# Performance work log

Measured on AMD Instinct MI355X. Metric: run time of the kernel, lower is better.

Reference implementation:

```python
import jax, jax.numpy as jnp
import numpy as np

# NOTE: the original source calls an undefined selective_scan_fn(x, delta, A_bar, B_bar, C)
# and returns y_proj(y). We implement the standard S6 diagonal selective scan it implies:
#   h_t = A_bar_t * h_{t-1} + B_bar_t * u_t   (elementwise over latent dim, h_0 = 0)
#   y_t = C_t * h_t
# with u = x_proj(x) (the only use of the otherwise-dangling x_proj in the source).

IN_CH = 96
OUT_CH = 96
LATENT = 256
BATCH, H, W = 2, 128, 128


def _linear(x, w, b):
    return x @ w.T + b


def _s6(x, xw, xb, bcw, bcb, dw, db, yw, yb):
    # x: [B, L, Cin]
    u = _linear(x, xw, xb)                      # [B, L, D]
    bc = _linear(x, bcw, bcb)                   # [B, L, 2D]
    delta = _linear(x, dw, db)                  # [B, L, D]
    Bm, Cm = jnp.split(bc, 2, axis=-1)
    A_bar = jnp.exp(-jax.nn.softplus(delta))    # in (0, 1)
    B_bar = (1.0 - A_bar) * Bm
    elems = (A_bar, B_bar * u)

    def combine(c1, c2):
        a1, b1 = c1
        a2, b2 = c2
        return (a1 * a2, a2 * b1 + b2)

    _, h = jax.lax.associative_scan(combine, elems, axis=1)  # parallel scan over L
    y = Cm * h
    return _linear(y, yw, yb)                   # [B, L, D]


def setup_inputs() -> dict:
    key = jax.random.key(0)
    ks = jax.random.split(key, 16)
    s = 0.02
    inp = {
        "x": jax.random.normal(ks[0], (BATCH, IN_CH, H, W), jnp.float32),
        # S6 params (shared across all 4 directional scans, as in the source)
        "xw": jax.random.normal(ks[1], (LATENT, IN_CH), jnp.float32) * s,
        "xb": jnp.zeros((LATENT,), jnp.float32),
        "bcw": jax.random.normal(ks[2], (2 * LATENT, IN_CH), jnp.float32) * s,
        "bcb": jnp.zeros((2 * LATENT,), jnp.float32),
        "dw": jax.random.normal(ks[3], (LATENT, IN_CH), jnp.float32) * s,
        "db": jnp.zeros((LATENT,), jnp.float32),
        "yw": jax.random.normal(ks[4], (LATENT, LATENT), jnp.float32) * s,
        "yb": jnp.zeros((LATENT,), jnp.float32),
        # CrossMerge params
        "mw": jax.random.normal(ks[5], (LATENT, 4 * LATENT), jnp.float32) * s,
        "mb": jnp.zeros((LATENT,), jnp.float32),
        "gw": jax.random.normal(ks[6], (LATENT, 4 * LATENT), jnp.float32) * s,
        "gb": jnp.zeros((LATENT,), jnp.float32),
        "ow": jax.random.normal(ks[7], (OUT_CH, LATENT), jnp.float32) * s,
        "ob": jnp.zeros((OUT_CH,), jnp.float32),
    }
    return inp


def reference(x, xw, xb, bcw, bcb, dw, db, yw, yb, mw, mb, gw, gb, ow, ob):
    B, C, Hh, Ww = x.shape
    # cross_scan: 4 directional flattenings
    s1 = x.transpose(0, 2, 3, 1).reshape(B, Hh * Ww, C)   # 'b c h w -> b (h w) c'
    s2 = x.transpose(0, 3, 2, 1).reshape(B, Ww * Hh, C)   # 'b c h w -> b (w h) c'
    s3 = s1[:, ::-1, :]
    s4 = s2[:, ::-1, :]
    p = (xw, xb, bcw, bcb, dw, db, yw, yb)
    y1 = _s6(s1, *p)
    y2 = _s6(s2, *p)
    y3 = _s6(s3, *p)
    y4 = _s6(s4, *p)
    # CrossMerge
    y_cat = jnp.concatenate([y1, y2, y3, y4], axis=-1)    # [B, L, 4D]
    y_merged = _linear(y_cat, mw, mb)
    gate = jax.nn.sigmoid(_linear(y_cat, gw, gb))
    out = _linear(y_merged * gate, ow, ob)                # [B, L, OUT_CH]
    # 'b (h w) c -> b c h w'
    return out.reshape(B, Hh, Ww, -1).transpose(0, 3, 1, 2)
```

## Files before the change

kernel.cpp:

```cpp
#include <hip/hip_runtime.h>
#include <stdint.h>

#define LL 16384
#define NB 2
#define CIN 96
#define NLAT 256
#define COUT 96
#define NCH 256
#define CHU 64

typedef __attribute__((ext_vector_type(8))) short short8v;
typedef __attribute__((ext_vector_type(4))) float float4v;

__device__ __forceinline__ float b2f(unsigned short h) {
    return __uint_as_float(((unsigned int)h) << 16);
}
__device__ __forceinline__ unsigned short f2b(float f) {
    unsigned int u = __float_as_uint(f);
    unsigned int r = (u + 0x7FFFu + ((u >> 16) & 1u)) >> 16;
    return (unsigned short)r;
}

#define GLL16(g, s) __builtin_amdgcn_global_load_lds( \
    (const __attribute__((address_space(1))) unsigned int*)(g), \
    (__attribute__((address_space(3))) unsigned int*)(s), 16, 0, 0)

__global__ __launch_bounds__(256) void k_foldw_part(
    const float* __restrict__ yw, const float* __restrict__ mw, const float* __restrict__ gw,
    float* __restrict__ WF)
{
    __shared__ float At[64][68];
    __shared__ float Bt[64][68];
    int jt = blockIdx.x, nt = blockIdx.y, dzk = blockIdx.z;
    int kc = dzk & 3, dz = dzk >> 2;
    int d = dz & 3, mat = dz >> 2;
    const float* src = mat ? gw : mw;
    int j0 = jt * 64, n0 = nt * 64;
    int tid = threadIdx.x, tx = tid & 15, ty = tid >> 4;
    float acc[4][4] = {};
    int i0 = kc * 64;
    for (int rep = 0; rep < 16; ++rep) {
        int idx = rep * 256 + tid;
        int r = idx >> 6, cq = idx & 63;
        At[r][cq] = yw[(size_t)(i0 + r) * 256 + j0 + cq];
        Bt[cq][r] = src[(size_t)(n0 + r) * 1024 + d * 256 + i0 + cq];
    }
    __syncthreads();
    for (int ii = 0; ii < 64; ++ii) {
        float4 a4 = *(const float4*)(&At[ii][ty * 4]);
        float4 b4 = *(const float4*)(&Bt[ii][tx * 4]);
        float av[4] = {a4.x, a4.y, a4.z, a4.w};
        float bv[4] = {b4.x, b4.y, b4.z, b4.w};
        for (int q = 0; q < 4; ++q)
            for (int p = 0; p < 4; ++p)
                acc[q][p] = fmaf(av[q], bv[p], acc[q][p]);
    }
    float* dst = WF + (size_t)kc * 512 * 1024;
    for (int q = 0; q < 4; ++q) {
        int k = d * 256 + j0 + ty * 4 + q;
        for (int p = 0; p < 4; ++p) {
            int n = n0 + tx * 4 + p;
            dst[(size_t)(mat * 256 + n) * 1024 + k] = acc[q][p];
        }
    }
}

__global__ __launch_bounds__(256) void k_foldsum(
    const float* __restrict__ WF, unsigned short* __restrict__ WBT)
{
    int t = blockIdx.x * 256 + threadIdx.x;
    size_t o = (size_t)t * 4;
    const size_t S = (size_t)512 * 1024;
    float4 s0 = *(const float4*)(WF + o);
    float4 s1 = *(const float4*)(WF + S + o);
    float4 s2 = *(const float4*)(WF + 2 * S + o);
    float4 s3 = *(const float4*)(WF + 3 * S + o);
    unsigned short pk[4];
    pk[0] = f2b(s0.x + s1.x + s2.x + s3.x);
    pk[1] = f2b(s0.y + s1.y + s2.y + s3.y);
    pk[2] = f2b(s0.z + s1.z + s2.z + s3.z);
    pk[3] = f2b(s0.w + s1.w + s2.w + s3.w);
    *(unsigned long long*)(&WBT[o]) = *(const unsigned long long*)pk;
}

__global__ void k_foldbias(const float* __restrict__ mw, const float* __restrict__ gw,
                           const float* __restrict__ mb, const float* __restrict__ gb,
                           const float* __restrict__ yb,
                           float* __restrict__ bm2, float* __restrict__ bg2)
{
    int row = blockIdx.x;
    int lane = threadIdx.x;
    int n = row & 255;
    const float* W = (row < 256) ? mw : gw;
    float s = 0.f;
    for (int k = lane; k < 1024; k += 64)
        s = fmaf(W[(size_t)n * 1024 + k], yb[k & 255], s);
    for (int off = 32; off; off >>= 1) s += __shfl_down(s, off);
    if (lane == 0) {
        if (row < 256) bm2[n] = s + mb[n];
        else           bg2[n] = s + gb[n];
    }
}

__global__ __launch_bounds__(256) void k_xpose(
    const float* __restrict__ x, unsigned short* __restrict__ XT)
{
    int t = threadIdx.x;
    int pl = t & 63;
    int grp = t >> 6;
    int p0 = blockIdx.x * 64;
    int b = p0 >> 14;
    int l = (p0 & (LL - 1)) + pl;
    size_t gp = (size_t)(p0 + pl);
    const float* xr = x + (size_t)b * 96 * LL + l;
    unsigned short* orow = XT + gp * 192;
#pragma unroll
    for (int kk = 0; kk < 3; ++kk) {
        int kq = grp * 3 + kk;
        short8v hi, lo;
#pragma unroll
        for (int c = 0; c < 8; ++c) {
            float v = xr[(size_t)(kq * 8 + c) * LL];
            unsigned short h = f2b(v);
            float r = v - b2f(h);
            hi[c] = (short)h;
            lo[c] = (short)f2b(r);
        }
        *(short8v*)(orow + kq * 8) = hi;
        *(short8v*)(orow + 96 + kq * 8) = lo;
    }
}

__global__ void k_wprep(
    const float* __restrict__ xw, const float* __restrict__ bcw, const float* __restrict__ dw,
    unsigned short* __restrict__ WPT)
{
    int rp = blockIdx.x * 32 + (threadIdx.x >> 3);
    int sub = threadIdx.x & 7;
    int nn16 = rp >> 6, g = (rp >> 4) & 3, ni = rp & 15;
    int n = nn16 * 16 + ni;
    const float* row;
    if (g == 0)      row = xw + (size_t)n * 96;
    else if (g == 1) row = bcw + (size_t)n * 96;
    else if (g == 2) row = bcw + (size_t)(256 + n) * 96;
    else             row = dw + (size_t)n * 96;
    unsigned short* orow = WPT + (size_t)rp * 192;
    for (int kq = sub; kq < 12; kq += 8) {
        short8v hv;
#pragma unroll
        for (int c = 0; c < 8; ++c) hv[c] = (short)f2b(row[kq * 8 + c]);
        *(short8v*)(orow + kq * 8) = hv;
        *(short8v*)(orow + 96 + kq * 8) = hv;
    }
}

__global__ void k_owprep(const float* __restrict__ ow, unsigned short* __restrict__ OWB)
{
    int r = blockIdx.x;
    int lane = threadIdx.x;
    unsigned short pk[4];
    if (r < 96) {
        float4 v = *(const float4*)(ow + (size_t)r * 256 + lane * 4);
        pk[0] = f2b(v.x); pk[1] = f2b(v.y); pk[2] = f2b(v.z); pk[3] = f2b(v.w);
    } else {
        pk[0] = pk[1] = pk[2] = pk[3] = 0;
    }
    *(unsigned long long*)(&OWB[(size_t)r * 256 + lane * 4]) = *(const unsigned long long*)pk;
}

__global__ __launch_bounds__(256) void k_proj_mfma(
    const unsigned short* __restrict__ XT, const unsigned short* __restrict__ WPT,
    const float* __restrict__ xb, const float* __restrict__ bcb, const float* __restrict__ db,
    unsigned int* __restrict__ AB, unsigned short* __restrict__ C)
{
    __shared__ __align__(16) unsigned short smA[128 * 32];
    __shared__ __align__(16) unsigned short smB[128 * 32];
    int tid = threadIdx.x;
    int w = tid >> 6, l = tid & 63;
    int mt = blockIdx.x;
    int bnt = blockIdx.y;
    int p0 = mt * 128;
    int bn0 = bnt * 128;

    int rowA = tid >> 2;
    int chA  = tid & 3;
    int laneRow = l & 15;
    int laneK   = l >> 4;

    float4v acc[2][8];
#pragma unroll
    for (int i = 0; i < 2; ++i)
#pragma unroll
        for (int f = 0; f < 8; ++f) acc[i][f] = (float4v)0.f;

    for (int kt = 0; kt < 6; ++kt) {
        const unsigned short* gA = XT + (size_t)(p0 + rowA) * 192 + kt * 32 + chA * 8;
        const unsigned short* gB = WPT + (size_t)(bn0 + rowA) * 192 + kt * 32 + chA * 8;
        GLL16(gA,            smA + tid * 8);
        GLL16(gA + 64 * 192, smA + 2048 + tid * 8);
        GLL16(gB,            smB + tid * 8);
        GLL16(gB + 64 * 192, smB + 2048 + tid * 8);
        __syncthreads();

        short8v a0 = *(const short8v*)(&smA[(w * 32 + laneRow) * 32 + laneK * 8]);
        short8v a1 = *(const short8v*)(&smA[(w * 32 + 16 + laneRow) * 32 + laneK * 8]);
#pragma unroll
        for (int f = 0; f < 8; ++f) {
            short8v bf_ = *(const short8v*)(&smB[(f * 16 + laneRow) * 32 + laneK * 8]);
            acc[0][f] = __builtin_amdgcn_mfma_f32_16x16x32_bf16(a0, bf_, acc[0][f], 0, 0, 0);
            acc[1][f] = __builtin_amdgcn_mfma_f32_16x16x32_bf16(a1, bf_, acc[1][f], 0, 0, 0);
        }
        __syncthreads();
    }

    int lr = l >> 4, lc = l & 15;
#pragma unroll
    for (int mr = 0; mr < 2; ++mr) {
#pragma unroll
        for (int nn2 = 0; nn2 < 2; ++nn2) {
            int n = (bnt * 2 + nn2) * 16 + lc;
            float xbv = xb[n], bb = bcb[n], cb = bcb[256 + n], dbv = db[n];
#pragma unroll
            for (int q = 0; q < 4; ++q) {
                int p = p0 + w * 32 + mr * 16 + lr * 4 + q;
                float u  = acc[mr][nn2 * 4 + 0][q] + xbv;
                float Bm = acc[mr][nn2 * 4 + 1][q] + bb;
                float Cm = acc[mr][nn2 * 4 + 2][q] + cb;
                float dl = acc[mr][nn2 * 4 + 3][q] + dbv;
                float a  = 1.0f / (1.0f + __expf(dl));
                float bu = (1.0f - a) * Bm * u;
                size_t base = (size_t)p * NLAT + n;
                AB[base] = (unsigned int)f2b(a) | ((unsigned int)f2b(bu) << 16);
                C[base]  = f2b(Cm);
            }
        }
    }
}

__device__ __forceinline__ int src_pos(int d, int t) {
    int s = (d >= 2) ? (LL - 1 - t) : t;
    return (d & 1) ? (((s & 127) << 7) | (s >> 7)) : s;
}

__global__ __launch_bounds__(256) void k_scan1(
    const unsigned int* __restrict__ AB,
    float* __restrict__ AggA, float* __restrict__ AggB)
{
    int n = threadIdx.x;
    int c = blockIdx.x, dp = blockIdx.y, b = blockIdx.z;
    int d1 = dp, d2 = dp + 2;
    int c2 = NCH - 1 - c;
    int t01 = c * CHU, t02 = c2 * CHU;
    const unsigned int* ABb = AB + (size_t)b * LL * NLAT + n;
    float h1 = 0.f, A1 = 1.f, h2 = 0.f, A2 = 1.f;
#pragma unroll 4
    for (int i = 0; i < CHU; ++i) {
        int ls1 = src_pos(d1, t01 + i);
        int ls2 = src_pos(d2, t02 + i);
        unsigned int v1 = ABb[(size_t)ls1 * NLAT];
        unsigned int v2 = ABb[(size_t)ls2 * NLAT];
        float a1 = __uint_as_float(v1 << 16), bu1 = __uint_as_float(v1 & 0xFFFF0000u);
        float a2 = __uint_as_float(v2 << 16), bu2 = __uint_as_float(v2 & 0xFFFF0000u);
        h1 = fmaf(a1, h1, bu1); A1 *= a1;
        h2 = fmaf(a2, h2, bu2); A2 *= a2;
    }
    size_t o1 = (((size_t)b * 4 + d1) * NCH + c) * NLAT + n;
    size_t o2 = (((size_t)b * 4 + d2) * NCH + c2) * NLAT + n;
    AggA[o1] = A1; AggB[o1] = h1;
    AggA[o2] = A2; AggB[o2] = h2;
}

__global__ void k_scan2(const float* __restrict__ AggA, const float* __restrict__ AggB,
                        float* __restrict__ Hs)
{
    int n = threadIdx.x;
    int d = blockIdx.x, b = blockIdx.y;
    float h = 0.f;
    for (int c = 0; c < NCH; ++c) {
        size_t o = (((size_t)b * 4 + d) * NCH + c) * NLAT + n;
        Hs[o] = h;
        h = fmaf(AggA[o], h, AggB[o]);
    }
}

__global__ __launch_bounds__(256) void k_scan3(
    const unsigned int* __restrict__ AB, const unsigned short* __restrict__ C,
    const float* __restrict__ Hs, unsigned short* __restrict__ ys)
{
    int n = threadIdx.x;
    int c = blockIdx.x, dp = blockIdx.y, b = blockIdx.z;
    int d1 = dp, d2 = dp + 2;
    int c2 = NCH - 1 - c;
    int t01 = c * CHU, t02 = c2 * CHU;
    const unsigned int* ABb = AB + (size_t)b * LL * NLAT + n;
    const unsigned short* Cb = C + (size_t)b * LL * NLAT + n;
    size_t o1 = (((size_t)b * 4 + d1) * NCH + c) * NLAT + n;
    size_t o2 = (((size_t)b * 4 + d2) * NCH + c2) * NLAT + n;
    float h1 = Hs[o1], h2 = Hs[o2];
    size_t yb1 = (((size_t)b * 4 + d1) * LL + t01) * NLAT + n;
    size_t yb2 = (((size_t)b * 4 + d2) * LL + t02) * NLAT + n;
#pragma unroll 4
    for (int i = 0; i < CHU; ++i) {
        int ls1 = src_pos(d1, t01 + i);
        int ls2 = src_pos(d2, t02 + i);
        size_t i1 = (size_t)ls1 * NLAT, i2 = (size_t)ls2 * NLAT;
        unsigned int v1 = ABb[i1];
        unsigned int v2 = ABb[i2];
        float a1 = __uint_as_float(v1 << 16), bu1 = __uint_as_float(v1 & 0xFFFF0000u);
        float a2 = __uint_as_float(v2 << 16), bu2 = __uint_as_float(v2 & 0xFFFF0000u);
        h1 = fmaf(a1, h1, bu1);
        h2 = fmaf(a2, h2, bu2);
        float y1 = b2f(Cb[i1]) * h1;
        float y2 = b2f(Cb[i2]) * h2;
        ys[yb1 + (size_t)i * NLAT] = f2b(y1);
        ys[yb2 + (size_t)i * NLAT] = f2b(y2);
    }
}

__global__ __launch_bounds__(256) void k_merge_mfma(
    const unsigned short* __restrict__ ys,
    const unsigned short* __restrict__ WBT,
    const float* __restrict__ bm2, const float* __restrict__ bg2,
    unsigned short* __restrict__ z)
{
    __shared__ __align__(16) unsigned short smA[2 * 128 * 32];
    __shared__ __align__(16) unsigned short smB[2 * 256 * 32];
    int tid = threadIdx.x;
    int w = tid >> 6, l = tid & 63;
    int wm = w >> 1, wn = w & 1;
    int mt = blockIdx.x;
    int nt = blockIdx.y;
    int p0 = mt * 128;
    int b4 = (p0 >> 14) * 4;
    int l0 = p0 & (LL - 1);
    int n0 = nt * 128;

    int rS = tid >> 2;
    int cg = (tid & 3) ^ ((rS >> 1) & 3);
    int laneRow = l & 15;
    int laneK   = l >> 4;
    int rx = (laneRow >> 1) & 3;

    float4v accM[4][4], accG[4][4];
#pragma unroll
    for (int i = 0; i < 4; ++i)
#pragma unroll
        for (int j = 0; j < 4; ++j) { accM[i][j] = (float4v)0.f; accG[i][j] = (float4v)0.f; }

    auto stage = [&](int kt, int buf) {
        int d = kt >> 3;
        int j0k = (kt & 7) * 32;
        const unsigned short* gAb = ys + (((size_t)(b4 + d)) * LL + l0) * 256 + j0k + cg * 8;
        unsigned short* sA = smA + buf * 4096;
        unsigned short* sB = smB + buf * 8192;
#pragma unroll
        for (int rep = 0; rep < 2; ++rep) {
            GLL16(gAb + (size_t)(rep * 64 + rS) * 256, sA + rep * 2048 + tid * 8);
        }
#pragma unroll
        for (int rep = 0; rep < 4; ++rep) {
            int rr = rep * 64 + rS;
            int nrow = (rr < 128) ? (n0 + rr) : (256 + n0 + rr - 128);
            GLL16(WBT + (size_t)nrow * 1024 + kt * 32 + cg * 8, sB + rep * 2048 + tid * 8);
        }
    };

    stage(0, 0);

    int cur = 0;
    for (int kt = 0; kt < 32; ++kt) {
        if (kt < 31) {
            stage(kt + 1, cur ^ 1);
            asm volatile("s_waitcnt vmcnt(6)" ::: "memory");
        } else {
            asm volatile("s_waitcnt vmcnt(0)" ::: "memory");
        }
        __builtin_amdgcn_s_barrier();

        const unsigned short* sA = smA + cur * 4096;
        const unsigned short* sB = smB + cur * 8192;
        int cxo = (laneK ^ rx) * 8;
        short8v a[4];
#pragma unroll
        for (int mr = 0; mr < 4; ++mr)
            a[mr] = *(const short8v*)(&sA[(wm * 64 + mr * 16 + laneRow) * 32 + cxo]);
#pragma unroll
        for (int nr = 0; nr < 4; ++nr) {
            short8v bm_ = *(const short8v*)(&sB[(wn * 64 + nr * 16 + laneRow) * 32 + cxo]);
            short8v bg_ = *(const short8v*)(&sB[(128 + wn * 64 + nr * 16 + laneRow) * 32 + cxo]);
#pragma unroll
            for (int mr = 0; mr < 4; ++mr) {
                accM[mr][nr] = __builtin_amdgcn_mfma_f32_16x16x32_bf16(a[mr], bm_, accM[mr][nr], 0, 0, 0);
                accG[mr][nr] = __builtin_amdgcn_mfma_f32_16x16x32_bf16(a[mr], bg_, accG[mr][nr], 0, 0, 0);
            }
        }
        __builtin_amdgcn_s_barrier();
        cur ^= 1;
    }

    int lr = l >> 4, lc = l & 15;
#pragma unroll
    for (int mr = 0; mr < 4; ++mr) {
#pragma unroll
        for (int nr = 0; nr < 4; ++nr) {
            int n = n0 + wn * 64 + nr * 16 + lc;
            float bmv = bm2[n], bgv = bg2[n];
#pragma unroll
            for (int q = 0; q < 4; ++q) {
                int p = p0 + wm * 64 + mr * 16 + lr * 4 + q;
                float m = accM[mr][nr][q] + bmv;
                float g = accG[mr][nr][q] + bgv;
                float zv = m / (1.f + __expf(-g));
                z[(size_t)p * NLAT + n] = f2b(zv);
            }
        }
    }
}

__global__ __launch_bounds__(256) void k_out_mfma(
    const unsigned short* __restrict__ z, const unsigned short* __restrict__ OWB,
    const float* __restrict__ ob, float* __restrict__ out)
{
    __shared__ __align__(16) unsigned short smA[128 * 32];
    __shared__ __align__(16) unsigned short smB[128 * 32];
    int tid = threadIdx.x;
    int w = tid >> 6, l = tid & 63;
    int p0 = blockIdx.x * 128;
    int b = p0 >> 14;
    int l0 = p0 & (LL - 1);

    int rowA = tid >> 2;
    int chA  = tid & 3;
    int laneRow = l & 15;
    int laneK   = l >> 4;

    float4v acc[2][6];
#pragma unroll
    for (int i = 0; i < 2; ++i)
#pragma unroll
        for (int f = 0; f < 6; ++f) acc[i][f] = (float4v)0.f;

    for (int kt = 0; kt < 8; ++kt) {
        const unsigned short* gA = z + (size_t)(p0 + rowA) * 256 + kt * 32 + chA * 8;
        const unsigned short* gB = OWB + (size_t)rowA * 256 + kt * 32 + chA * 8;
        GLL16(gA,            smA + tid * 8);
        GLL16(gA + 64 * 256, smA + 2048 + tid * 8);
        GLL16(gB,            smB + tid * 8);
        GLL16(gB + 64 * 256, smB + 2048 + tid * 8);
        __syncthreads();

        short8v a0 = *(const short8v*)(&smA[(w * 32 + laneRow) * 32 + laneK * 8]);
        short8v a1 = *(const short8v*)(&smA[(w * 32 + 16 + laneRow) * 32 + laneK * 8]);
#pragma unroll
        for (int nr = 0; nr < 6; ++nr) {
            short8v bf_ = *(const short8v*)(&smB[(nr * 16 + laneRow) * 32 + laneK * 8]);
            acc[0][nr] = __builtin_amdgcn_mfma_f32_16x16x32_bf16(a0, bf_, acc[0][nr], 0, 0, 0);
            acc[1][nr] = __builtin_amdgcn_mfma_f32_16x16x32_bf16(a1, bf_, acc[1][nr], 0, 0, 0);
        }
        __syncthreads();
    }

    int lr = l >> 4, lc = l & 15;
#pragma unroll
    for (int mr = 0; mr < 2; ++mr) {
#pragma unroll
        for (int nr = 0; nr < 6; ++nr) {
            int c = nr * 16 + lc;
            float obv = ob[c];
            int ll = l0 + w * 32 + mr * 16 + lr * 4;
            float4 v;
            v.x = acc[mr][nr][0] + obv;
            v.y = acc[mr][nr][1] + obv;
            v.z = acc[mr][nr][2] + obv;
            v.w = acc[mr][nr][3] + obv;
            *(float4*)(&out[((size_t)(b * 96 + c)) * LL + ll]) = v;
        }
    }
}

extern "C" void kernel_launch(void* const* d_in, const int* in_sizes, int n_in,
                              void* d_out, int out_size, void* d_ws, size_t ws_size,
                              hipStream_t stream) {
    (void)in_sizes; (void)n_in; (void)out_size; (void)ws_size;
    const float* x   = (const float*)d_in[0];
    const float* xw  = (const float*)d_in[1];
    const float* xb  = (const float*)d_in[2];
    const float* bcw = (const float*)d_in[3];
    const float* bcb = (const float*)d_in[4];
    const float* dw  = (const float*)d_in[5];
    const float* db  = (const float*)d_in[6];
    const float* yw  = (const float*)d_in[7];
    const float* yb  = (const float*)d_in[8];
    const float* mw  = (const float*)d_in[9];
    const float* mb  = (const float*)d_in[10];
    const float* gw  = (const float*)d_in[11];
    const float* gb  = (const float*)d_in[12];
    const float* ow  = (const float*)d_in[13];
    const float* ob  = (const float*)d_in[14];
    float* out = (float*)d_out;

    char* ws = (char*)d_ws;
    size_t off = 0;
    auto alloc = [&](size_t bytes) -> void* {
        void* p = ws + off;
        off += (bytes + 255) & ~(size_t)255;
        return p;
    };
    unsigned int*   AB  = (unsigned int*)  alloc((size_t)NB * LL * NLAT * 4);
    unsigned short* C   = (unsigned short*)alloc((size_t)NB * LL * NLAT * 2);
    unsigned short* YS  = (unsigned short*)alloc((size_t)NB * 4 * LL * NLAT * 2);
    unsigned short* Z   = (unsigned short*)alloc((size_t)NB * LL * NLAT * 2);
    unsigned short* WBT = (unsigned short*)alloc((size_t)512 * 1024 * 2);
    unsigned short* XT  = (unsigned short*)alloc((size_t)NB * LL * 192 * 2);
    unsigned short* WPT = (unsigned short*)alloc((size_t)1024 * 192 * 2);
    unsigned short* OWB = (unsigned short*)alloc((size_t)128 * 256 * 2);
    float* WF   = (float*)alloc((size_t)4 * 512 * 1024 * 4);
    float* BM2  = (float*)alloc(256 * 4);
    float* BG2  = (float*)alloc(256 * 4);
    float* AggA = (float*)alloc((size_t)NB * 4 * NCH * NLAT * 4);
    float* AggB = (float*)alloc((size_t)NB * 4 * NCH * NLAT * 4);
    float* HS   = (float*)alloc((size_t)NB * 4 * NCH * NLAT * 4);

    k_foldw_part<<<dim3(4, 4, 32),   256, 0, stream>>>(yw, mw, gw, WF);
    k_foldsum   <<<512,              256, 0, stream>>>(WF, WBT);
    k_foldbias  <<<512,               64, 0, stream>>>(mw, gw, mb, gb, yb, BM2, BG2);
    k_wprep     <<<32,               256, 0, stream>>>(xw, bcw, dw, WPT);
    k_owprep    <<<128,               64, 0, stream>>>(ow, OWB);
    k_xpose     <<<512,              256, 0, stream>>>(x, XT);
    k_proj_mfma <<<dim3(256, 8),     256, 0, stream>>>(XT, WPT, xb, bcb, db, AB, C);
    k_scan1     <<<dim3(NCH, 2, NB), 256, 0, stream>>>(AB, AggA, AggB);
    k_scan2     <<<dim3(4, NB),      256, 0, stream>>>(AggA, AggB, HS);
    k_scan3     <<<dim3(NCH, 2, NB), 256, 0, stream>>>(AB, C, HS, YS);
    k_merge_mfma<<<dim3(256, 2),     256, 0, stream>>>(YS, WBT, BM2, BG2, Z);
    k_out_mfma  <<<256,              256, 0, stream>>>(Z, OWB, ob, out);
}
```

Baseline: 189.5 us.

## Merge prep kernels into one launch and parallelize chunk-carry scan

Four small preprocessing kernels (input transpose/split, projection weight prep, output weight prep, bias folding) are combined into one kernel that branches on block index, cutting three launches. The middle scan stage, which ran only 8 blocks with each thread looping serially over 256 chunks, now runs one block per (latent, direction, batch) and does a Hillis-Steele scan in shared memory. The new scan reads AggA/AggB with a stride of NLAT floats between threads, so its loads are uncoalesced, and it does log-depth work with many barriers.

```diff
diff --git a/kernel.cpp b/kernel.cpp
--- a/kernel.cpp
+++ b/kernel.cpp
@@ -83,89 +83,88 @@
     *(unsigned long long*)(&WBT[o]) = *(const unsigned long long*)pk;
 }
 
-__global__ void k_foldbias(const float* __restrict__ mw, const float* __restrict__ gw,
-                           const float* __restrict__ mb, const float* __restrict__ gb,
-                           const float* __restrict__ yb,
-                           float* __restrict__ bm2, float* __restrict__ bg2)
-{
-    int row = blockIdx.x;
-    int lane = threadIdx.x;
-    int n = row & 255;
-    const float* W = (row < 256) ? mw : gw;
-    float s = 0.f;
-    for (int k = lane; k < 1024; k += 64)
-        s = fmaf(W[(size_t)n * 1024 + k], yb[k & 255], s);
-    for (int off = 32; off; off >>= 1) s += __shfl_down(s, off);
-    if (lane == 0) {
-        if (row < 256) bm2[n] = s + mb[n];
-        else           bg2[n] = s + gb[n];
-    }
-}
-
-__global__ __launch_bounds__(256) void k_xpose(
-    const float* __restrict__ x, unsigned short* __restrict__ XT)
-{
+__global__ __launch_bounds__(256) void k_prep(
+    const float* __restrict__ x, unsigned short* __restrict__ XT,
+    const float* __restrict__ xw, const float* __restrict__ bcw, const float* __restrict__ dw,
+    unsigned short* __restrict__ WPT,
+    const float* __restrict__ ow, unsigned short* __restrict__ OWB,
+    const float* __restrict__ mw, const float* __restrict__ gw,
+    const float* __restrict__ mb, const float* __restrict__ gb,
+    const float* __restrict__ yb,
+    float* __restrict__ bm2, float* __restrict__ bg2)
+{
+    int bid = blockIdx.x;
     int t = threadIdx.x;
-    int pl = t & 63;
-    int grp = t >> 6;
-    int p0 = blockIdx.x * 64;
-    int b = p0 >> 14;
-    int l = (p0 & (LL - 1)) + pl;
-    size_t gp = (size_t)(p0 + pl);
-    const float* xr = x + (size_t)b * 96 * LL + l;
-    unsigned short* orow = XT + gp * 192;
-#pragma unroll
-    for (int kk = 0; kk < 3; ++kk) {
-        int kq = grp * 3 + kk;
-        short8v hi, lo;
-#pragma unroll
-        for (int c = 0; c < 8; ++c) {
-            float v = xr[(size_t)(kq * 8 + c) * LL];
-            unsigned short h = f2b(v);
-            float r = v - b2f(h);
-            hi[c] = (short)h;
-            lo[c] = (short)f2b(r);
-        }
-        *(short8v*)(orow + kq * 8) = hi;
-        *(short8v*)(orow + 96 + kq * 8) = lo;
-    }
-}
-
-__global__ void k_wprep(
-    const float* __restrict__ xw, const float* __restrict__ bcw, const float* __restrict__ dw,
-    unsigned short* __restrict__ WPT)
-{
-    int rp = blockIdx.x * 32 + (threadIdx.x >> 3);
-    int sub = threadIdx.x & 7;
-    int nn16 = rp >> 6, g = (rp >> 4) & 3, ni = rp & 15;
-    int n = nn16 * 16 + ni;
-    const float* row;
-    if (g == 0)      row = xw + (size_t)n * 96;
-    else if (g == 1) row = bcw + (size_t)n * 96;
-    else if (g == 2) row = bcw + (size_t)(256 + n) * 96;
-    else             row = dw + (size_t)n * 96;
-    unsigned short* orow = WPT + (size_t)rp * 192;
-    for (int kq = sub; kq < 12; kq += 8) {
-        short8v hv;
-#pragma unroll
-        for (int c = 0; c < 8; ++c) hv[c] = (short)f2b(row[kq * 8 + c]);
-        *(short8v*)(orow + kq * 8) = hv;
-        *(short8v*)(orow + 96 + kq * 8) = hv;
-    }
-}
-
-__global__ void k_owprep(const float* __restrict__ ow, unsigned short* __restrict__ OWB)
-{
-    int r = blockIdx.x;
-    int lane = threadIdx.x;
-    unsigned short pk[4];
-    if (r < 96) {
-        float4 v = *(const float4*)(ow + (size_t)r * 256 + lane * 4);
-        pk[0] = f2b(v.x); pk[1] = f2b(v.y); pk[2] = f2b(v.z); pk[3] = f2b(v.w);
+    if (bid < 512) {
+        int pl = t & 63;
+        int grp = t >> 6;
+        int p0 = bid * 64;
+        int b = p0 >> 14;
+        int l = (p0 & (LL - 1)) + pl;
+        size_t gp = (size_t)(p0 + pl);
+        const float* xr = x + (size_t)b * 96 * LL + l;
+        unsigned short* orow = XT + gp * 192;
+#pragma unroll
+        for (int kk = 0; kk < 3; ++kk) {
+            int kq = grp * 3 + kk;
+            short8v hi, lo;
+#pragma unroll
+            for (int c = 0; c < 8; ++c) {
+                float v = xr[(size_t)(kq * 8 + c) * LL];
+                unsigned short h = f2b(v);
+                float r = v - b2f(h);
+                hi[c] = (short)h;
+                lo[c] = (short)f2b(r);
+            }
+            *(short8v*)(orow + kq * 8) = hi;
+            *(short8v*)(orow + 96 + kq * 8) = lo;
+        }
+    } else if (bid < 544) {
+        int unit = bid - 512;
+        int rp = unit * 32 + (t >> 3);
+        int sub = t & 7;
+        int nn16 = rp >> 6, g = (rp >> 4) & 3, ni = rp & 15;
+        int n = nn16 * 16 + ni;
+        const float* row;
+        if (g == 0)      row = xw + (size_t)n * 96;
+        else if (g == 1) row = bcw + (size_t)n * 96;
+        else if (g == 2) row = bcw + (size_t)(256 + n) * 96;
+        else             row = dw + (size_t)n * 96;
+        unsigned short* orow = WPT + (size_t)rp * 192;
+        for (int kq = sub; kq < 12; kq += 8) {
+            short8v hv;
+#pragma unroll
+            for (int c = 0; c < 8; ++c) hv[c] = (short)f2b(row[kq * 8 + c]);
+            *(short8v*)(orow + kq * 8) = hv;
+            *(short8v*)(orow + 96 + kq * 8) = hv;
+        }
+    } else if (bid < 576) {
+        int unit = bid - 544;
+        int r = unit * 4 + (t >> 6);
+        int lane = t & 63;
+        unsigned short pk[4];
+        if (r < 96) {
+            float4 v = *(const float4*)(ow + (size_t)r * 256 + lane * 4);
+            pk[0] = f2b(v.x); pk[1] = f2b(v.y); pk[2] = f2b(v.z); pk[3] = f2b(v.w);
+        } else {
+            pk[0] = pk[1] = pk[2] = pk[3] = 0;
+        }
+        *(unsigned long long*)(&OWB[(size_t)r * 256 + lane * 4]) = *(const unsigned long long*)pk;
     } else {
-        pk[0] = pk[1] = pk[2] = pk[3] = 0;
-    }
-    *(unsigned long long*)(&OWB[(size_t)r * 256 + lane * 4]) = *(const unsigned long long*)pk;
+        int unit = bid - 576;
+        int row = unit * 4 + (t >> 6);
+        int lane = t & 63;
+        int n = row & 255;
+        const float* W = (row < 256) ? mw : gw;
+        float s = 0.f;
+        for (int k = lane; k < 1024; k += 64)
+            s = fmaf(W[(size_t)n * 1024 + k], yb[k & 255], s);
+        for (int off = 32; off; off >>= 1) s += __shfl_down(s, off);
+        if (lane == 0) {
+            if (row < 256) bm2[n] = s + mb[n];
+            else           bg2[n] = s + gb[n];
+        }
+    }
 }
 
 __global__ __launch_bounds__(256) void k_proj_mfma(
@@ -270,17 +269,32 @@
     AggA[o2] = A2; AggB[o2] = h2;
 }
 
-__global__ void k_scan2(const float* __restrict__ AggA, const float* __restrict__ AggB,
-                        float* __restrict__ Hs)
-{
-    int n = threadIdx.x;
-    int d = blockIdx.x, b = blockIdx.y;
-    float h = 0.f;
-    for (int c = 0; c < NCH; ++c) {
-        size_t o = (((size_t)b * 4 + d) * NCH + c) * NLAT + n;
-        Hs[o] = h;
-        h = fmaf(AggA[o], h, AggB[o]);
-    }
+__global__ __launch_bounds__(256) void k_scan2(
+    const float* __restrict__ AggA, const float* __restrict__ AggB,
+    float* __restrict__ Hs)
+{
+    __shared__ float sA[NCH];
+    __shared__ float sB[NCH];
+    int n = blockIdx.x;
+    int d = blockIdx.y, b = blockIdx.z;
+    int c = threadIdx.x;
+    size_t o = (((size_t)b * 4 + d) * NCH + c) * NLAT + n;
+    sA[c] = AggA[o];
+    sB[c] = AggB[o];
+    __syncthreads();
+#pragma unroll
+    for (int st = 1; st < NCH; st <<= 1) {
+        float pA = 1.f, pB = 0.f;
+        if (c >= st) { pA = sA[c - st]; pB = sB[c - st]; }
+        __syncthreads();
+        if (c >= st) {
+            float aO = sA[c];
+            sB[c] = fmaf(aO, pB, sB[c]);
+            sA[c] = aO * pA;
+        }
+        __syncthreads();
+    }
+    Hs[o] = (c == 0) ? 0.f : sB[c - 1];
 }
 
 __global__ __launch_bounds__(256) void k_scan3(
@@ -521,16 +535,14 @@
     float* AggB = (float*)alloc((size_t)NB * 4 * NCH * NLAT * 4);
     float* HS   = (float*)alloc((size_t)NB * 4 * NCH * NLAT * 4);
 
-    k_foldw_part<<<dim3(4, 4, 32),   256, 0, stream>>>(yw, mw, gw, WF);
-    k_foldsum   <<<512,              256, 0, stream>>>(WF, WBT);
-    k_foldbias  <<<512,               64, 0, stream>>>(mw, gw, mb, gb, yb, BM2, BG2);
-    k_wprep     <<<32,               256, 0, stream>>>(xw, bcw, dw, WPT);
-    k_owprep    <<<128,               64, 0, stream>>>(ow, OWB);
-    k_xpose     <<<512,              256, 0, stream>>>(x, XT);
-    k_proj_mfma <<<dim3(256, 8),     256, 0, stream>>>(XT, WPT, xb, bcb, db, AB, C);
-    k_scan1     <<<dim3(NCH, 2, NB), 256, 0, stream>>>(AB, AggA, AggB);
-    k_scan2     <<<dim3(4, NB),      256, 0, stream>>>(AggA, AggB, HS);
-    k_scan3     <<<dim3(NCH, 2, NB), 256, 0, stream>>>(AB, C, HS, YS);
-    k_merge_mfma<<<dim3(256, 2),     256, 0, stream>>>(YS, WBT, BM2, BG2, Z);
-    k_out_mfma  <<<256,              256, 0, stream>>>(Z, OWB, ob, out);
-}
+    k_foldw_part<<<dim3(4, 4, 32),    256, 0, stream>>>(yw, mw, gw, WF);
+    k_foldsum   <<<512,               256, 0, stream>>>(WF, WBT);
+    k_prep      <<<704,               256, 0, stream>>>(x, XT, xw, bcw, dw, WPT,
+                                                        ow, OWB, mw, gw, mb, gb, yb, BM2, BG2);
+    k_proj_mfma <<<dim3(256, 8),      256, 0, stream>>>(XT, WPT, xb, bcb, db, AB, C);
+    k_scan1     <<<dim3(NCH, 2, NB),  256, 0, stream>>>(AB, AggA, AggB);
+    k_scan2     <<<dim3(NLAT, 4, NB), 256, 0, stream>>>(AggA, AggB, HS);
+    k_scan3     <<<dim3(NCH, 2, NB),  256, 0, stream>>>(AB, C, HS, YS);
+    k_merge_mfma<<<dim3(256, 2),      256, 0, stream>>>(YS, WBT, BM2, BG2, Z);
+    k_out_mfma  <<<256,               256, 0, stream>>>(Z, OWB, ob, out);
+}
```

Result: faster. 177.5 us (-6.3%).
